# Kernel tuning notes

Hardware: AMD Instinct MI355X
Metric: run time of the kernel (lower is better)

Reference implementation:

```python
import jax, jax.numpy as jnp
import numpy as np

N_NODES = 50000
N_EDGES = 800000
IN_DIM, HID_DIM, OUT_DIM = 128, 128, 64


def _sage_conv(x, src, dst, W_l, W_r, b, num_nodes):
    # mean aggregation of source-node features onto destination nodes
    msg = x[src]  # [E, d] gather
    summed = jax.ops.segment_sum(msg, dst, num_segments=num_nodes)  # [N, d]
    deg = jax.ops.segment_sum(jnp.ones((src.shape[0],), dtype=x.dtype), dst,
                              num_segments=num_nodes)  # [N]
    agg = summed / jnp.maximum(deg, 1.0)[:, None]
    # SAGEConv: lin_l(agg) + lin_r(x); bias only on lin_l (PyG default)
    return agg @ W_l + b + x @ W_r


def setup_inputs() -> dict:
    key = jax.random.key(0)
    k = jax.random.split(key, 8)
    def glorot(kk, shape):
        lim = float(np.sqrt(6.0 / (shape[0] + shape[1])))
        return jax.random.uniform(kk, shape, jnp.float32, -lim, lim)
    return {
        "x": jax.random.normal(k[0], (N_NODES, IN_DIM), jnp.float32),
        "edge_index": jax.random.randint(k[1], (2, N_EDGES), 0, N_NODES, jnp.int64),
        "W1_l": glorot(k[2], (IN_DIM, HID_DIM)),
        "W1_r": glorot(k[3], (IN_DIM, HID_DIM)),
        "b1": jnp.zeros((HID_DIM,), jnp.float32),
        "W2_l": glorot(k[4], (HID_DIM, OUT_DIM)),
        "W2_r": glorot(k[5], (HID_DIM, OUT_DIM)),
        "b2": jnp.zeros((OUT_DIM,), jnp.float32),
    }


def reference(x, edge_index, W1_l, W1_r, b1, W2_l, W2_r, b2):
    src, dst = edge_index[0], edge_index[1]
    n = x.shape[0]
    h = _sage_conv(x, src, dst, W1_l, W1_r, b1, n)
    h = jax.nn.relu(h)
    # dropout is identity in eval mode
    out = _sage_conv(h, src, dst, W2_l, W2_r, b2, n)
    return out
```

## Files before the change

kernel.cpp:

```cpp
#include <hip/hip_runtime.h>
#include <hip/hip_bf16.h>


#define BLK 256

typedef __attribute__((ext_vector_type(8))) short short8;
typedef __attribute__((ext_vector_type(4))) float f32x4;

__device__ inline unsigned short f2bf(float f) {
    unsigned int u = __builtin_bit_cast(unsigned int, f);
    u += 0x7fffu + ((u >> 16) & 1u);
    return (unsigned short)(u >> 16);
}
__device__ inline float bf2f(unsigned short h) {
    return __builtin_bit_cast(float, ((unsigned int)h) << 16);
}


__global__ __launch_bounds__(BLK) void deg_count_kernel(const int* __restrict__ dst,
                                                        int E, int* __restrict__ deg) {
    int e = blockIdx.x * BLK + threadIdx.x;
    if (e < E) atomicAdd(&deg[dst[e]], 1);
}

__global__ __launch_bounds__(BLK) void partial_sum_kernel(const int* __restrict__ deg,
                                                          int n, int* __restrict__ partials) {
    __shared__ int s[BLK];
    int t = threadIdx.x;
    int idx = blockIdx.x * BLK + t;
    s[t] = (idx < n) ? deg[idx] : 0;
    __syncthreads();
    for (int o = BLK / 2; o > 0; o >>= 1) {
        if (t < o) s[t] += s[t + o];
        __syncthreads();
    }
    if (t == 0) partials[blockIdx.x] = s[0];
}

__global__ __launch_bounds__(BLK) void scan_partials_kernel(int* __restrict__ partials, int n) {
    __shared__ int s[BLK];
    int t = threadIdx.x;
    int v = (t < n) ? partials[t] : 0;
    s[t] = v;
    __syncthreads();
    int sum = v;
    for (int o = 1; o < BLK; o <<= 1) {
        int other = (t >= o) ? s[t - o] : 0;
        __syncthreads();
        sum += other;
        s[t] = sum;
        __syncthreads();
    }
    if (t < n) partials[t] = sum - v;
}

__global__ __launch_bounds__(BLK) void chunk_scan_kernel(const int* __restrict__ deg,
                                                         const int* __restrict__ partials,
                                                         int n, int* __restrict__ row_start) {
    __shared__ int s[BLK];
    int t = threadIdx.x;
    int idx = blockIdx.x * BLK + t;
    int v = (idx < n) ? deg[idx] : 0;
    s[t] = v;
    __syncthreads();
    int sum = v;
    for (int o = 1; o < BLK; o <<= 1) {
        int other = (t >= o) ? s[t - o] : 0;
        __syncthreads();
        sum += other;
        s[t] = sum;
        __syncthreads();
    }
    if (idx < n) row_start[idx] = (sum - v) + partials[blockIdx.x];
}

__global__ __launch_bounds__(BLK) void fill_kernel(const int* __restrict__ src,
                                                   const int* __restrict__ dst, int E,
                                                   const int* __restrict__ row_start,
                                                   int* __restrict__ cursor,
                                                   int* __restrict__ csr_src) {
    int e = blockIdx.x * BLK + threadIdx.x;
    if (e >= E) return;
    int d = dst[e];
    int pos = atomicAdd(&cursor[d], 1);
    atomicExch(&csr_src[row_start[d] + pos], src[e]);
}


__global__ __launch_bounds__(BLK) void f32_to_bf16_kernel(const float* __restrict__ in,
                                                          unsigned short* __restrict__ out,
                                                          int nquad) {
    int i = blockIdx.x * BLK + threadIdx.x;
    if (i >= nquad) return;
    float4 v = ((const float4*)in)[i];
    ushort4 o;
    o.x = f2bf(v.x); o.y = f2bf(v.y); o.z = f2bf(v.z); o.w = f2bf(v.w);
    ((ushort4*)out)[i] = o;
}

__global__ __launch_bounds__(BLK) void pack_all_w_kernel(const float* __restrict__ W1l,
                                                         const float* __restrict__ W1r,
                                                         const float* __restrict__ W2l,
                                                         const float* __restrict__ W2r,
                                                         unsigned short* __restrict__ P1l,
                                                         unsigned short* __restrict__ P1r,
                                                         unsigned short* __restrict__ P2l,
                                                         unsigned short* __restrict__ P2r) {
    int t = blockIdx.x * BLK + threadIdx.x;
    const float* W;
    unsigned short* P;
    int Ncol, local;
    if (t < 16384)      { W = W1l; P = P1l; Ncol = 128; local = t; }
    else if (t < 32768) { W = W1r; P = P1r; Ncol = 128; local = t - 16384; }
    else if (t < 40960) { W = W2l; P = P2l; Ncol = 64;  local = t - 32768; }
    else if (t < 49152) { W = W2r; P = P2r; Ncol = 64;  local = t - 40960; }
    else return;
    int j = local & 7;
    int lane = (local >> 3) & 63;
    int rest = local >> 9;
    int nt = Ncol >> 4;
    int n16 = rest % nt, kb = rest / nt;
    int k = kb * 32 + (lane >> 4) * 8 + j;
    int c = n16 * 16 + (lane & 15);
    P[local] = f2bf(W[(size_t)k * Ncol + c]);
}


__global__ __launch_bounds__(BLK) void agg_bf16_kernel(const unsigned short* __restrict__ feat,
                                                       const int* __restrict__ row_start,
                                                       const int* __restrict__ deg,
                                                       const int* __restrict__ csr_src,
                                                       unsigned short* __restrict__ out,
                                                       int n_nodes) {
    int gid = blockIdx.x * (BLK / 64) + (threadIdx.x >> 6);
    int lane = threadIdx.x & 63;
    if (gid >= n_nodes) return;
    int start = row_start[gid];
    int cnt = deg[gid];
    const unsigned int* fp = (const unsigned int*)feat;
    float ax[8], ay[8];
#pragma unroll
    for (int j = 0; j < 8; j++) { ax[j] = 0.f; ay[j] = 0.f; }

    for (int base = 0; base < cnt; base += 64) {
        int rem = cnt - base;
        int m = rem < 64 ? rem : 64;
        int idx = csr_src[start + base + (lane < m ? lane : m - 1)];
        int e = 0;
        for (; e + 8 <= m; e += 8) {
            unsigned int v[8];
#pragma unroll
            for (int j = 0; j < 8; j++) {
                int s = __shfl(idx, e + j);
                v[j] = fp[(size_t)s * 64 + lane];
            }
#pragma unroll
            for (int j = 0; j < 8; j++) {
                ax[j] += bf2f((unsigned short)v[j]);
                ay[j] += bf2f((unsigned short)(v[j] >> 16));
            }
        }
        for (; e < m; ++e) {
            int s = __shfl(idx, e);
            unsigned int v = fp[(size_t)s * 64 + lane];
            ax[0] += bf2f((unsigned short)v);
            ay[0] += bf2f((unsigned short)(v >> 16));
        }
    }
    float sx = ((ax[0] + ax[1]) + (ax[2] + ax[3])) + ((ax[4] + ax[5]) + (ax[6] + ax[7]));
    float sy = ((ay[0] + ay[1]) + (ay[2] + ay[3])) + ((ay[4] + ay[5]) + (ay[6] + ay[7]));
    float inv = 1.0f / fmaxf((float)cnt, 1.0f);
    unsigned int packed = (unsigned int)f2bf(sx * inv) | ((unsigned int)f2bf(sy * inv) << 16);
    ((unsigned int*)out)[(size_t)gid * 64 + lane] = packed;
}


template <int NCOL, bool RELU, bool OUT_BF16>
__global__ __launch_bounds__(BLK) void gemm_mfma_kernel(const unsigned short* __restrict__ A1,
                                                        const unsigned short* __restrict__ A2,
                                                        const unsigned short* __restrict__ Pl,
                                                        const unsigned short* __restrict__ Pr,
                                                        const float* __restrict__ bias,
                                                        void* __restrict__ outp, int M) {
    constexpr int NT = NCOL / 16;
    const int wave = threadIdx.x >> 6, lane = threadIdx.x & 63;
    const int r0 = blockIdx.x * 128 + wave * 32;
    const int arow = lane & 15, kgrp = lane >> 4;

    f32x4 acc[2][NT];
#pragma unroll
    for (int h = 0; h < 2; h++)
#pragma unroll
        for (int n = 0; n < NT; n++) acc[h][n] = (f32x4){0.f, 0.f, 0.f, 0.f};

    const int ra = min(r0 + arow, M - 1);
    const int rb = min(r0 + 16 + arow, M - 1);

#pragma unroll
    for (int mat = 0; mat < 2; ++mat) {
        const unsigned short* A = mat ? A2 : A1;
        const unsigned short* P = mat ? Pr : Pl;
        const unsigned short* Aa = A + (size_t)ra * 128 + kgrp * 8;
        const unsigned short* Ab = A + (size_t)rb * 128 + kgrp * 8;
#pragma unroll
        for (int kb = 0; kb < 4; ++kb) {
            short8 afa = *(const short8*)(Aa + kb * 32);
            short8 afb = *(const short8*)(Ab + kb * 32);
            const unsigned short* Pk = P + (size_t)kb * NT * 512 + lane * 8;
#pragma unroll
            for (int n = 0; n < NT; ++n) {
                short8 wf = *(const short8*)(Pk + n * 512);
                acc[0][n] = __builtin_amdgcn_mfma_f32_16x16x32_bf16(afa, wf, acc[0][n], 0, 0, 0);
                acc[1][n] = __builtin_amdgcn_mfma_f32_16x16x32_bf16(afb, wf, acc[1][n], 0, 0, 0);
            }
        }
    }

#pragma unroll
    for (int n = 0; n < NT; ++n) {
        int col = n * 16 + arow;
        float bv = bias[col];
#pragma unroll
        for (int h = 0; h < 2; ++h) {
#pragma unroll
            for (int i = 0; i < 4; ++i) {
                int row = r0 + h * 16 + kgrp * 4 + i;
                if (row < M) {
                    float v = acc[h][n][i] + bv;
                    if (RELU) v = fmaxf(v, 0.f);
                    if (OUT_BF16)
                        ((unsigned short*)outp)[(size_t)row * NCOL + col] = f2bf(v);
                    else
                        ((float*)outp)[(size_t)row * NCOL + col] = v;
                }
            }
        }
    }
}


extern "C" void kernel_launch(void* const* d_in, const int* in_sizes, int n_in,
                              void* d_out, int out_size, void* d_ws, size_t ws_size,
                              hipStream_t stream) {
    const float* x   = (const float*)d_in[0];
    const int*   ei  = (const int*)d_in[1];
    const float* W1l = (const float*)d_in[2];
    const float* W1r = (const float*)d_in[3];
    const float* b1  = (const float*)d_in[4];
    const float* W2l = (const float*)d_in[5];
    const float* W2r = (const float*)d_in[6];
    const float* b2  = (const float*)d_in[7];
    float* out = (float*)d_out;

    const int N = in_sizes[0] / 128;
    const int E = in_sizes[1] / 2;
    const int* src = ei;
    const int* dst = ei + E;

    char* ws = (char*)d_ws;
    size_t off = 0;
    auto carve = [&](size_t bytes) {
        void* p = ws + off;
        off += (bytes + 255) & ~(size_t)255;
        return p;
    };
    int* deg       = (int*)carve((size_t)2 * N * 4);
    int* cursor    = deg + N;
    int* row_start = (int*)carve((size_t)N * 4);
    int* partials  = (int*)carve(256 * 4);
    int* csr_src   = (int*)carve((size_t)E * 4);
    unsigned short* xb   = (unsigned short*)carve((size_t)N * 128 * 2);
    unsigned short* aggb = (unsigned short*)carve((size_t)N * 128 * 2);
    unsigned short* hb   = (unsigned short*)carve((size_t)N * 128 * 2);
    unsigned short* P1l  = (unsigned short*)carve(128 * 128 * 2);
    unsigned short* P1r  = (unsigned short*)carve(128 * 128 * 2);
    unsigned short* P2l  = (unsigned short*)carve(128 * 64 * 2);
    unsigned short* P2r  = (unsigned short*)carve(128 * 64 * 2);

    hipMemsetAsync(deg, 0, (size_t)2 * N * 4, stream);

    const int nquad = N * 128 / 4;
    f32_to_bf16_kernel<<<(nquad + BLK - 1) / BLK, BLK, 0, stream>>>(x, xb, nquad);
    pack_all_w_kernel<<<192, BLK, 0, stream>>>(W1l, W1r, W2l, W2r, P1l, P1r, P2l, P2r);

    const int nchunk = (N + BLK - 1) / BLK;
    deg_count_kernel<<<(E + BLK - 1) / BLK, BLK, 0, stream>>>(dst, E, deg);
    partial_sum_kernel<<<nchunk, BLK, 0, stream>>>(deg, N, partials);
    scan_partials_kernel<<<1, BLK, 0, stream>>>(partials, nchunk);
    chunk_scan_kernel<<<nchunk, BLK, 0, stream>>>(deg, partials, N, row_start);
    fill_kernel<<<(E + BLK - 1) / BLK, BLK, 0, stream>>>(src, dst, E, row_start, cursor, csr_src);

    const int aggGrid = (N + 3) / 4;
    const int gemmGrid = (N + 127) / 128;

    agg_bf16_kernel<<<aggGrid, BLK, 0, stream>>>(xb, row_start, deg, csr_src, aggb, N);
    gemm_mfma_kernel<128, true, true><<<gemmGrid, BLK, 0, stream>>>(aggb, xb, P1l, P1r, b1, hb, N);
    agg_bf16_kernel<<<aggGrid, BLK, 0, stream>>>(hb, row_start, deg, csr_src, aggb, N);
    gemm_mfma_kernel<64, false, false><<<gemmGrid, BLK, 0, stream>>>(aggb, hb, P2l, P2r, b2, out, N);
}
```

Before: 303.8 us.

## Project before aggregating in layer 2, range-partition CSR fill, widen gather unroll

Layer 2 now applies W2_l to h first (a 64-wide projection), then mean-aggregates the 64-wide result with a new half-wave gather kernel. A fused GEMM applies W2_r, adds the aggregated projection and the bias, and writes the output. This halves the bytes gathered per edge in the second aggregation. The CSR fill runs in four passes, each handling one destination range, and uses plain stores instead of atomicExch. The aim is better locality on the atomics, at the cost of reading the edge list four times. The layer-1 gather loop is also unrolled to 16 loads in flight, and the extra bf16 rounding of the projected features may slightly change accuracy.

New measurement: 325.7 us. 7.2% more time.

```diff
diff --git a/kernel.cpp b/kernel.cpp
--- a/kernel.cpp
+++ b/kernel.cpp
@@ -74,16 +74,18 @@
     if (idx < n) row_start[idx] = (sum - v) + partials[blockIdx.x];
 }
 
-__global__ __launch_bounds__(BLK) void fill_kernel(const int* __restrict__ src,
-                                                   const int* __restrict__ dst, int E,
-                                                   const int* __restrict__ row_start,
-                                                   int* __restrict__ cursor,
-                                                   int* __restrict__ csr_src) {
+__global__ __launch_bounds__(BLK) void fill_range_kernel(const int* __restrict__ src,
+                                                         const int* __restrict__ dst, int E,
+                                                         const int* __restrict__ row_start,
+                                                         int* __restrict__ cursor,
+                                                         int* __restrict__ csr_src,
+                                                         int lo, int hi) {
     int e = blockIdx.x * BLK + threadIdx.x;
     if (e >= E) return;
     int d = dst[e];
+    if (d < lo || d >= hi) return;
     int pos = atomicAdd(&cursor[d], 1);
-    atomicExch(&csr_src[row_start[d] + pos], src[e]);
+    csr_src[row_start[d] + pos] = src[e];
 }
 
 
@@ -126,12 +128,12 @@
 }
 
 
-__global__ __launch_bounds__(BLK) void agg_bf16_kernel(const unsigned short* __restrict__ feat,
-                                                       const int* __restrict__ row_start,
-                                                       const int* __restrict__ deg,
-                                                       const int* __restrict__ csr_src,
-                                                       unsigned short* __restrict__ out,
-                                                       int n_nodes) {
+__global__ __launch_bounds__(BLK) void agg128_kernel(const unsigned short* __restrict__ feat,
+                                                     const int* __restrict__ row_start,
+                                                     const int* __restrict__ deg,
+                                                     const int* __restrict__ csr_src,
+                                                     unsigned short* __restrict__ out,
+                                                     int n_nodes) {
     int gid = blockIdx.x * (BLK / 64) + (threadIdx.x >> 6);
     int lane = threadIdx.x & 63;
     if (gid >= n_nodes) return;
@@ -147,17 +149,17 @@
         int m = rem < 64 ? rem : 64;
         int idx = csr_src[start + base + (lane < m ? lane : m - 1)];
         int e = 0;
-        for (; e + 8 <= m; e += 8) {
-            unsigned int v[8];
-#pragma unroll
-            for (int j = 0; j < 8; j++) {
+        for (; e + 16 <= m; e += 16) {
+            unsigned int v[16];
+#pragma unroll
+            for (int j = 0; j < 16; j++) {
                 int s = __shfl(idx, e + j);
                 v[j] = fp[(size_t)s * 64 + lane];
             }
 #pragma unroll
-            for (int j = 0; j < 8; j++) {
-                ax[j] += bf2f((unsigned short)v[j]);
-                ay[j] += bf2f((unsigned short)(v[j] >> 16));
+            for (int j = 0; j < 16; j++) {
+                ax[j & 7] += bf2f((unsigned short)v[j]);
+                ay[j & 7] += bf2f((unsigned short)(v[j] >> 16));
             }
         }
         for (; e < m; ++e) {
@@ -175,8 +177,65 @@
 }
 
 
+__global__ __launch_bounds__(BLK) void agg64_kernel(const unsigned short* __restrict__ feat,
+                                                    const int* __restrict__ row_start,
+                                                    const int* __restrict__ deg,
+                                                    const int* __restrict__ csr_src,
+                                                    unsigned short* __restrict__ out,
+                                                    int n_nodes) {
+    int gid = blockIdx.x * (BLK / 64) + (threadIdx.x >> 6);
+    int lane = threadIdx.x & 63;
+    int hi = lane >> 5, lane31 = lane & 31;
+    if (gid >= n_nodes) return;
+    int start = row_start[gid];
+    int cnt = deg[gid];
+    const unsigned int* fp = (const unsigned int*)feat;
+    float ax[8], ay[8];
+#pragma unroll
+    for (int j = 0; j < 8; j++) { ax[j] = 0.f; ay[j] = 0.f; }
+
+    for (int base = 0; base < cnt; base += 64) {
+        int rem = cnt - base;
+        int m = rem < 64 ? rem : 64;
+        int idx = csr_src[start + base + (lane < m ? lane : m - 1)];
+        int e = 0;
+        for (; e + 32 <= m; e += 32) {
+            unsigned int v[16];
+#pragma unroll
+            for (int j = 0; j < 16; j++) {
+                int s = __shfl(idx, e + 2 * j + hi);
+                v[j] = fp[(size_t)s * 32 + lane31];
+            }
+#pragma unroll
+            for (int j = 0; j < 16; j++) {
+                ax[j & 7] += bf2f((unsigned short)v[j]);
+                ay[j & 7] += bf2f((unsigned short)(v[j] >> 16));
+            }
+        }
+        for (; e < m; e += 2) {
+            int eb = e + hi;
+            if (eb < m) {
+                int s = __shfl(idx, eb);
+                unsigned int v = fp[(size_t)s * 32 + lane31];
+                ax[0] += bf2f((unsigned short)v);
+                ay[0] += bf2f((unsigned short)(v >> 16));
+            }
+        }
+    }
+    float sx = ((ax[0] + ax[1]) + (ax[2] + ax[3])) + ((ax[4] + ax[5]) + (ax[6] + ax[7]));
+    float sy = ((ay[0] + ay[1]) + (ay[2] + ay[3])) + ((ay[4] + ay[5]) + (ay[6] + ay[7]));
+    sx += __shfl_xor(sx, 32);
+    sy += __shfl_xor(sy, 32);
+    if (hi == 0) {
+        float inv = 1.0f / fmaxf((float)cnt, 1.0f);
+        unsigned int packed = (unsigned int)f2bf(sx * inv) | ((unsigned int)f2bf(sy * inv) << 16);
+        ((unsigned int*)out)[(size_t)gid * 32 + lane31] = packed;
+    }
+}
+
+
 template <int NCOL, bool RELU, bool OUT_BF16>
-__global__ __launch_bounds__(BLK) void gemm_mfma_kernel(const unsigned short* __restrict__ A1,
+__global__ __launch_bounds__(BLK) void gemm_dual_kernel(const unsigned short* __restrict__ A1,
                                                         const unsigned short* __restrict__ A2,
                                                         const unsigned short* __restrict__ Pl,
                                                         const unsigned short* __restrict__ Pr,
@@ -232,6 +291,120 @@
                         ((unsigned short*)outp)[(size_t)row * NCOL + col] = f2bf(v);
                     else
                         ((float*)outp)[(size_t)row * NCOL + col] = v;
+                }
+            }
+        }
+    }
+}
+
+template <int NCOL>
+__global__ __launch_bounds__(BLK) void gemm_single_kernel(const unsigned short* __restrict__ A,
+                                                          const unsigned short* __restrict__ P,
+                                                          unsigned short* __restrict__ outp,
+                                                          int M) {
+    constexpr int NT = NCOL / 16;
+    const int wave = threadIdx.x >> 6, lane = threadIdx.x & 63;
+    const int r0 = blockIdx.x * 128 + wave * 32;
+    const int arow = lane & 15, kgrp = lane >> 4;
+
+    f32x4 acc[2][NT];
+#pragma unroll
+    for (int h = 0; h < 2; h++)
+#pragma unroll
+        for (int n = 0; n < NT; n++) acc[h][n] = (f32x4){0.f, 0.f, 0.f, 0.f};
+
+    const int ra = min(r0 + arow, M - 1);
+    const int rb = min(r0 + 16 + arow, M - 1);
+    const unsigned short* Aa = A + (size_t)ra * 128 + kgrp * 8;
+    const unsigned short* Ab = A + (size_t)rb * 128 + kgrp * 8;
+#pragma unroll
+    for (int kb = 0; kb < 4; ++kb) {
+        short8 afa = *(const short8*)(Aa + kb * 32);
+        short8 afb = *(const short8*)(Ab + kb * 32);
+        const unsigned short* Pk = P + (size_t)kb * NT * 512 + lane * 8;
+#pragma unroll
+        for (int n = 0; n < NT; ++n) {
+            short8 wf = *(const short8*)(Pk + n * 512);
+            acc[0][n] = __builtin_amdgcn_mfma_f32_16x16x32_bf16(afa, wf, acc[0][n], 0, 0, 0);
+            acc[1][n] = __builtin_amdgcn_mfma_f32_16x16x32_bf16(afb, wf, acc[1][n], 0, 0, 0);
+        }
+    }
+
+#pragma unroll
+    for (int n = 0; n < NT; ++n) {
+        int col = n * 16 + arow;
+#pragma unroll
+        for (int h = 0; h < 2; ++h) {
+#pragma unroll
+            for (int i = 0; i < 4; ++i) {
+                int row = r0 + h * 16 + kgrp * 4 + i;
+                if (row < M)
+                    outp[(size_t)row * NCOL + col] = f2bf(acc[h][n][i]);
+            }
+        }
+    }
+}
+
+template <int NCOL>
+__global__ __launch_bounds__(BLK) void gemm_add_kernel(const unsigned short* __restrict__ A,
+                                                       const unsigned short* __restrict__ P,
+                                                       const unsigned short* __restrict__ AGG,
+                                                       const float* __restrict__ bias,
+                                                       float* __restrict__ outp, int M) {
+    constexpr int NT = NCOL / 16;
+    __shared__ unsigned int sAgg[128 * NCOL / 2];
+    const int wave = threadIdx.x >> 6, lane = threadIdx.x & 63;
+    const int r0 = blockIdx.x * 128 + wave * 32;
+    const int r0blk = blockIdx.x * 128;
+    const int arow = lane & 15, kgrp = lane >> 4;
+
+    const unsigned int* aggp = (const unsigned int*)AGG;
+#pragma unroll
+    for (int i = 0; i < (128 * NCOL / 2) / BLK; ++i) {
+        int id = threadIdx.x + BLK * i;
+        int row = id / (NCOL / 2), cu = id % (NCOL / 2);
+        int g = min(r0blk + row, M - 1);
+        sAgg[id] = aggp[(size_t)g * (NCOL / 2) + cu];
+    }
+    __syncthreads();
+
+    f32x4 acc[2][NT];
+#pragma unroll
+    for (int h = 0; h < 2; h++)
+#pragma unroll
+        for (int n = 0; n < NT; n++) acc[h][n] = (f32x4){0.f, 0.f, 0.f, 0.f};
+
+    const int ra = min(r0 + arow, M - 1);
+    const int rb = min(r0 + 16 + arow, M - 1);
+    const unsigned short* Aa = A + (size_t)ra * 128 + kgrp * 8;
+    const unsigned short* Ab = A + (size_t)rb * 128 + kgrp * 8;
+#pragma unroll
+    for (int kb = 0; kb < 4; ++kb) {
+        short8 afa = *(const short8*)(Aa + kb * 32);
+        short8 afb = *(const short8*)(Ab + kb * 32);
+        const unsigned short* Pk = P + (size_t)kb * NT * 512 + lane * 8;
+#pragma unroll
+        for (int n = 0; n < NT; ++n) {
+            short8 wf = *(const short8*)(Pk + n * 512);
+            acc[0][n] = __builtin_amdgcn_mfma_f32_16x16x32_bf16(afa, wf, acc[0][n], 0, 0, 0);
+            acc[1][n] = __builtin_amdgcn_mfma_f32_16x16x32_bf16(afb, wf, acc[1][n], 0, 0, 0);
+        }
+    }
+
+    const unsigned short* sA16 = (const unsigned short*)sAgg;
+#pragma unroll
+    for (int n = 0; n < NT; ++n) {
+        int col = n * 16 + arow;
+        float bv = bias[col];
+#pragma unroll
+        for (int h = 0; h < 2; ++h) {
+#pragma unroll
+            for (int i = 0; i < 4; ++i) {
+                int lrow = wave * 32 + h * 16 + kgrp * 4 + i;
+                int row = r0blk + lrow;
+                if (row < M) {
+                    float v = acc[h][n][i] + bv + bf2f(sA16[lrow * NCOL + col]);
+                    outp[(size_t)row * NCOL + col] = v;
                 }
             }
         }
@@ -276,6 +449,8 @@
     unsigned short* P1r  = (unsigned short*)carve(128 * 128 * 2);
     unsigned short* P2l  = (unsigned short*)carve(128 * 64 * 2);
     unsigned short* P2r  = (unsigned short*)carve(128 * 64 * 2);
+    unsigned short* pb   = xb;
+    unsigned short* aggp = aggb;
 
     hipMemsetAsync(deg, 0, (size_t)2 * N * 4, stream);
 
@@ -288,13 +463,22 @@
     partial_sum_kernel<<<nchunk, BLK, 0, stream>>>(deg, N, partials);
     scan_partials_kernel<<<1, BLK, 0, stream>>>(partials, nchunk);
     chunk_scan_kernel<<<nchunk, BLK, 0, stream>>>(deg, partials, N, row_start);
-    fill_kernel<<<(E + BLK - 1) / BLK, BLK, 0, stream>>>(src, dst, E, row_start, cursor, csr_src);
+
+    const int PASSES = 4;
+    const int range = (N + PASSES - 1) / PASSES;
+    for (int p = 0; p < PASSES; ++p) {
+        int lo = p * range;
+        int hic = min(N, lo + range);
+        fill_range_kernel<<<(E + BLK - 1) / BLK, BLK, 0, stream>>>(src, dst, E, row_start,
+                                                                   cursor, csr_src, lo, hic);
+    }
 
     const int aggGrid = (N + 3) / 4;
     const int gemmGrid = (N + 127) / 128;
 
-    agg_bf16_kernel<<<aggGrid, BLK, 0, stream>>>(xb, row_start, deg, csr_src, aggb, N);
-    gemm_mfma_kernel<128, true, true><<<gemmGrid, BLK, 0, stream>>>(aggb, xb, P1l, P1r, b1, hb, N);
-    agg_bf16_kernel<<<aggGrid, BLK, 0, stream>>>(hb, row_start, deg, csr_src, aggb, N);
-    gemm_mfma_kernel<64, false, false><<<gemmGrid, BLK, 0, stream>>>(aggb, hb, P2l, P2r, b2, out, N);
-}
+    agg128_kernel<<<aggGrid, BLK, 0, stream>>>(xb, row_start, deg, csr_src, aggb, N);
+    gemm_dual_kernel<128, true, true><<<gemmGrid, BLK, 0, stream>>>(aggb, xb, P1l, P1r, b1, hb, N);
+    gemm_single_kernel<64><<<gemmGrid, BLK, 0, stream>>>(hb, P2l, pb, N);
+    agg64_kernel<<<aggGrid, BLK, 0, stream>>>(pb, row_start, deg, csr_src, aggp, N);
+    gemm_add_kernel<64><<<gemmGrid, BLK, 0, stream>>>(hb, P2r, aggp, b2, out, N);
+}
```
